# Kernel optimization log

Measured on AMD Instinct MI355X. Metric: run time of the kernel, lower is better.

The kernel has to match this reference:

```python
import jax, jax.numpy as jnp
import numpy as np

E = 8        # num_experts
D_IN = 512   # num_inputs
H = 256      # num_neurons_expert
T = 64       # num_neurons_tower
B = 16384    # batch


def setup_inputs() -> dict:
    key = jax.random.key(0)
    ks = jax.random.split(key, 7)
    s_in = 1.0 / np.sqrt(D_IN)
    s_h = 1.0 / np.sqrt(H)
    return {
        "xv": jax.random.normal(ks[0], (B, D_IN), dtype=jnp.float32),
        # expert weights stacked: torch Linear weight is (out,in) -> (E, H, D_IN)
        "We": jax.random.uniform(ks[1], (E, H, D_IN), jnp.float32, -s_in, s_in),
        "be": jax.random.uniform(ks[2], (E, H), jnp.float32, -s_in, s_in),
        "Wg": jax.random.uniform(ks[3], (E, D_IN), jnp.float32, -s_in, s_in),
        "bg": jax.random.uniform(ks[4], (E,), jnp.float32, -s_in, s_in),
        "Wt": jax.random.uniform(ks[5], (T, H), jnp.float32, -s_h, s_h),
        "bt": jax.random.uniform(ks[6], (T,), jnp.float32, -s_h, s_h),
    }


def reference(xv, We, be, Wg, bg, Wt, bt):
    # All experts as one batched GEMM: [B,D] x [E,H,D] -> [B,E,H]
    experts = jax.nn.relu(jnp.einsum("bd,ehd->beh", xv, We) + be[None, :, :])
    # Dropout is identity in eval mode.
    gate = jax.nn.softmax(xv @ Wg.T + bg, axis=1)            # [B,E]
    combined = jnp.einsum("beh,be->bh", experts, gate)        # [B,H]
    out = jax.nn.sigmoid(combined @ Wt.T + bt)                # [B,T]
    return out
```

## Files before the change

kernel.cpp:

```cpp
#include <hip/hip_runtime.h>
#include <hip/hip_bf16.h>
#include <stdint.h>

typedef unsigned short u16;
typedef __bf16 bf16x8 __attribute__((ext_vector_type(8)));
typedef float f32x4 __attribute__((ext_vector_type(4)));


__device__ __forceinline__ void glds16(const void* g, void* l) {
  __builtin_amdgcn_global_load_lds(
      (const __attribute__((address_space(1))) unsigned int*)g,
      (__attribute__((address_space(3))) unsigned int*)l, 16, 0, 0);
}

__device__ __forceinline__ u16 f2bf(float f) {
  unsigned int u = __builtin_bit_cast(unsigned int, f);
  u += 0x7fffu + ((u >> 16) & 1u);
  return (u16)(u >> 16);
}

__global__ __launch_bounds__(256) void prep_w(
    const float* __restrict__ We, const float* __restrict__ Wt,
    const float* __restrict__ Wg,
    u16* __restrict__ We_bf, u16* __restrict__ Wt_bf,
    u16* __restrict__ Wg_hi, u16* __restrict__ Wg_lo) {
  const int bx = blockIdx.x;
  if (bx < 520) {
    const float* src; u16* dst;
    if (bx < 512) { int base = bx * 2048 + threadIdx.x * 8; src = We + base; dst = We_bf + base; }
    else { int base = (bx - 512) * 2048 + threadIdx.x * 8; src = Wt + base; dst = Wt_bf + base; }
    float4 a = *(const float4*)src;
    float4 b = *(const float4*)(src + 4);
    uint4 o;
    o.x = (unsigned)f2bf(a.x) | ((unsigned)f2bf(a.y) << 16);
    o.y = (unsigned)f2bf(a.z) | ((unsigned)f2bf(a.w) << 16);
    o.z = (unsigned)f2bf(b.x) | ((unsigned)f2bf(b.y) << 16);
    o.w = (unsigned)f2bf(b.z) | ((unsigned)f2bf(b.w) << 16);
    *(uint4*)dst = o;
  } else {
    int base = (bx - 520) * 2048 + threadIdx.x * 8;
    float x[8];
    float4 a = *(const float4*)(Wg + base);
    float4 b = *(const float4*)(Wg + base + 4);
    x[0]=a.x; x[1]=a.y; x[2]=a.z; x[3]=a.w; x[4]=b.x; x[5]=b.y; x[6]=b.z; x[7]=b.w;
    u16 h[8], l[8];
#pragma unroll
    for (int j = 0; j < 8; j++) {
      h[j] = f2bf(x[j]);
      float hf = __builtin_bit_cast(float, ((unsigned)h[j]) << 16);
      l[j] = f2bf(x[j] - hf);
    }
    uint4 oh, ol;
    oh.x = (unsigned)h[0] | ((unsigned)h[1] << 16);
    oh.y = (unsigned)h[2] | ((unsigned)h[3] << 16);
    oh.z = (unsigned)h[4] | ((unsigned)h[5] << 16);
    oh.w = (unsigned)h[6] | ((unsigned)h[7] << 16);
    ol.x = (unsigned)l[0] | ((unsigned)l[1] << 16);
    ol.y = (unsigned)l[2] | ((unsigned)l[3] << 16);
    ol.z = (unsigned)l[4] | ((unsigned)l[5] << 16);
    ol.w = (unsigned)l[6] | ((unsigned)l[7] << 16);
    *(uint4*)(Wg_hi + base) = oh;
    *(uint4*)(Wg_lo + base) = ol;
  }
}

__device__ __forceinline__ void stage_chunk(const u16* __restrict__ We_bf,
                                            u16* ldsbuf, int t, int tid) {
  const int e_ = t >> 3, kc_ = t & 7;
  const u16* src = We_bf + (e_ << 17) + (kc_ << 6);
#pragma unroll
  for (int r = 0; r < 8; r++) {
    int gi = r * 256 + tid;
    int n = gi >> 3, s = gi & 7;
    int g = s ^ (n & 7);
    glds16(src + (n << 9) + (g << 3), ldsbuf + (gi << 3));
  }
}

__global__ __launch_bounds__(256, 2) void moe_main(
    const float* __restrict__ xv, const u16* __restrict__ We_bf,
    const float* __restrict__ be, const float* __restrict__ bg,
    const u16* __restrict__ Wg_hi, const u16* __restrict__ Wg_lo,
    const u16* __restrict__ Wt_bf, const float* __restrict__ bt,
    float* __restrict__ out) {
  __shared__ u16 lds[36864];
  float* beL = (float*)&lds[32768];

  const int tid = threadIdx.x;
  const int lane = tid & 63;
  const int wid = tid >> 6;
  const int wn = wid;
  const int l15 = lane & 15;
  const int l4 = lane >> 4;
  const int m0 = blockIdx.x << 5;

  stage_chunk(We_bf, lds, 0, tid);
  *(float4*)(beL + (tid << 3)) = *(const float4*)(be + (tid << 3));
  *(float4*)(beL + (tid << 3) + 4) = *(const float4*)(be + (tid << 3) + 4);
  stage_chunk(We_bf, &lds[16384], 1, tid);

  bf16x8 ah[2][16];
  f32x4 g0[2] = {{0.f,0.f,0.f,0.f},{0.f,0.f,0.f,0.f}};
  f32x4 g1[2] = {{0.f,0.f,0.f,0.f},{0.f,0.f,0.f,0.f}};
  f32x4 g2[2] = {{0.f,0.f,0.f,0.f},{0.f,0.f,0.f,0.f}};
  const int esrc = l15 & 7;
#pragma unroll
  for (int mt = 0; mt < 2; mt++) {
#pragma unroll
    for (int ks = 0; ks < 16; ks++) {
      const float* ap = xv + ((m0 + mt * 16 + l15) << 9) + ks * 32 + l4 * 8;
      float4 xa = *(const float4*)ap;
      float4 xb = *(const float4*)(ap + 4);
      float x[8];
      x[0]=xa.x; x[1]=xa.y; x[2]=xa.z; x[3]=xa.w; x[4]=xb.x; x[5]=xb.y; x[6]=xb.z; x[7]=xb.w;
      bf16x8 hv, lv;
#pragma unroll
      for (int j = 0; j < 8; j++) {
        u16 hb_ = f2bf(x[j]);
        float hf = __builtin_bit_cast(float, ((unsigned)hb_) << 16);
        hv[j] = __builtin_bit_cast(__bf16, hb_);
        lv[j] = __builtin_bit_cast(__bf16, f2bf(x[j] - hf));
      }
      ah[mt][ks] = hv;
      bf16x8 wh = *(const bf16x8*)(Wg_hi + (esrc << 9) + ks * 32 + l4 * 8);
      bf16x8 wl = *(const bf16x8*)(Wg_lo + (esrc << 9) + ks * 32 + l4 * 8);
      g0[mt] = __builtin_amdgcn_mfma_f32_16x16x32_bf16(hv, wh, g0[mt], 0, 0, 0);
      g1[mt] = __builtin_amdgcn_mfma_f32_16x16x32_bf16(lv, wh, g1[mt], 0, 0, 0);
      g2[mt] = __builtin_amdgcn_mfma_f32_16x16x32_bf16(hv, wl, g2[mt], 0, 0, 0);
    }
  }
  float gv[2][4];
  {
    float bgv = bg[esrc];
#pragma unroll
    for (int mt = 0; mt < 2; mt++)
#pragma unroll
      for (int i = 0; i < 4; i++) {
        float z = g0[mt][i] + g1[mt][i] + g2[mt][i] + bgv;
        float mx = z;
        mx = fmaxf(mx, __shfl_xor(mx, 1));
        mx = fmaxf(mx, __shfl_xor(mx, 2));
        mx = fmaxf(mx, __shfl_xor(mx, 4));
        float p = __expf(z - mx);
        float s = p;
        s += __shfl_xor(s, 1);
        s += __shfl_xor(s, 2);
        s += __shfl_xor(s, 4);
        gv[mt][i] = p / s;
      }
  }

  f32x4 comb[2][4];
#pragma unroll
  for (int mt = 0; mt < 2; mt++)
#pragma unroll
    for (int nt = 0; nt < 4; nt++) comb[mt][nt] = {0.f, 0.f, 0.f, 0.f};

#pragma unroll 1
  for (int e = 0; e < 8; e++) {
    f32x4 acc[2][4];
#pragma unroll
    for (int mt = 0; mt < 2; mt++)
#pragma unroll
      for (int nt = 0; nt < 4; nt++) acc[mt][nt] = {0.f, 0.f, 0.f, 0.f};

#pragma unroll
    for (int kc = 0; kc < 8; kc++) {
      int t = e * 8 + kc;
      __syncthreads();
      if (t + 1 >= 2 && t + 1 < 64)
        stage_chunk(We_bf, &lds[((t & 1) ^ 1) << 14], t + 1, tid);
      const u16* ldsB = &lds[(t & 1) << 14];
#pragma unroll
      for (int ks = 0; ks < 2; ks++) {
        bf16x8 bfr[4];
#pragma unroll
        for (int nt = 0; nt < 4; nt++) {
          int n = wn * 64 + nt * 16 + l15;
          int g = ks * 4 + l4;
          int slot = g ^ (n & 7);
          bfr[nt] = *(const bf16x8*)&ldsB[(n << 6) + (slot << 3)];
        }
#pragma unroll
        for (int mt = 0; mt < 2; mt++)
#pragma unroll
          for (int nt = 0; nt < 4; nt++)
            acc[mt][nt] = __builtin_amdgcn_mfma_f32_16x16x32_bf16(
                ah[mt][kc * 2 + ks], bfr[nt], acc[mt][nt], 0, 0, 0);
      }
    }
    float bev[4];
#pragma unroll
    for (int nt = 0; nt < 4; nt++)
      bev[nt] = beL[(e << 8) + wn * 64 + nt * 16 + l15];
#pragma unroll
    for (int mt = 0; mt < 2; mt++)
#pragma unroll
      for (int i = 0; i < 4; i++) {
        float g = __shfl(gv[mt][i], (lane & 48) | e);
#pragma unroll
        for (int nt = 0; nt < 4; nt++)
          comb[mt][nt][i] += g * fmaxf(acc[mt][nt][i] + bev[nt], 0.f);
      }
  }

#pragma unroll
  for (int mt = 0; mt < 2; mt++)
#pragma unroll
    for (int i = 0; i < 4; i++) {
      int row = mt * 16 + l4 * 4 + i;
#pragma unroll
      for (int nt = 0; nt < 4; nt++) {
        int col = wn * 64 + nt * 16 + l15;
        __bf16 v = (__bf16)comb[mt][nt][i];
        lds[row * 264 + col] = __builtin_bit_cast(u16, v);
      }
    }
  __syncthreads();
  if (wid < 2) {
    f32x4 tacc[4];
#pragma unroll
    for (int nt = 0; nt < 4; nt++) tacc[nt] = {0.f, 0.f, 0.f, 0.f};
#pragma unroll
    for (int ks = 0; ks < 8; ks++) {
      bf16x8 aT = *(const bf16x8*)&lds[(wid * 16 + l15) * 264 + ks * 32 + l4 * 8];
#pragma unroll
      for (int nt = 0; nt < 4; nt++) {
        bf16x8 bT = *(const bf16x8*)&Wt_bf[(nt * 16 + l15) * 256 + ks * 32 + l4 * 8];
        tacc[nt] = __builtin_amdgcn_mfma_f32_16x16x32_bf16(aT, bT, tacc[nt], 0, 0, 0);
      }
    }
#pragma unroll
    for (int nt = 0; nt < 4; nt++) {
      float btv = bt[nt * 16 + l15];
#pragma unroll
      for (int i = 0; i < 4; i++) {
        int row = m0 + wid * 16 + l4 * 4 + i;
        float v = tacc[nt][i] + btv;
        out[row * 64 + nt * 16 + l15] = 1.f / (1.f + __expf(-v));
      }
    }
  }
}

extern "C" void kernel_launch(void* const* d_in, const int* in_sizes, int n_in,
                              void* d_out, int out_size, void* d_ws, size_t ws_size,
                              hipStream_t stream) {
  const float* xv = (const float*)d_in[0];
  const float* We = (const float*)d_in[1];
  const float* be = (const float*)d_in[2];
  const float* Wg = (const float*)d_in[3];
  const float* bg = (const float*)d_in[4];
  const float* Wt = (const float*)d_in[5];
  const float* bt = (const float*)d_in[6];

  char* ws = (char*)d_ws;
  u16* We_bf = (u16*)ws;
  u16* Wt_bf = (u16*)(ws + 2097152);
  u16* Wg_hi = (u16*)(ws + 2129920);
  u16* Wg_lo = (u16*)(ws + 2138112);

  prep_w<<<522, 256, 0, stream>>>(We, Wt, Wg, We_bf, Wt_bf, Wg_hi, Wg_lo);
  moe_main<<<512, 256, 0, stream>>>(xv, We_bf, be, bg, Wg_hi, Wg_lo, Wt_bf, bt,
                                    (float*)d_out);
}
```

Before: 177.9 us.

## Triple-buffer half-size We chunks with vmcnt barriers and stage A fragments in LDS

Splits each We K-chunk into two 128-row halves and cycles them through a three-slot LDS ring. Full __syncthreads are replaced with s_waitcnt vmcnt(4)+s_barrier, so one chunk's loads stay in flight during compute. The bf16 x fragments (ah[2][16]) move from registers into a swizzled LDS tile written by wave 0, freeing VGPRs for occupancy. In exchange, A operands are now reloaded from LDS every k-step, and be is read from global memory instead of LDS.

Result: faster. 152.7 us (-14.1%).

```diff
diff --git a/kernel.cpp b/kernel.cpp
--- a/kernel.cpp
+++ b/kernel.cpp
@@ -6,6 +6,9 @@
 typedef __bf16 bf16x8 __attribute__((ext_vector_type(8)));
 typedef float f32x4 __attribute__((ext_vector_type(4)));
 
+
+#define BAR_V4 asm volatile("s_waitcnt vmcnt(4)\ns_barrier" ::: "memory")
+#define BAR_V0 asm volatile("s_waitcnt vmcnt(0)\ns_barrier" ::: "memory")
 
 __device__ __forceinline__ void glds16(const void* g, void* l) {
   __builtin_amdgcn_global_load_lds(
@@ -65,15 +68,15 @@
 }
 
 __device__ __forceinline__ void stage_chunk(const u16* __restrict__ We_bf,
-                                            u16* ldsbuf, int t, int tid) {
-  const int e_ = t >> 3, kc_ = t & 7;
-  const u16* src = We_bf + (e_ << 17) + (kc_ << 6);
-#pragma unroll
-  for (int r = 0; r < 8; r++) {
+                                            u16* buf, int t, int tid) {
+  const int e_ = t >> 4, kc_ = (t >> 1) & 7, half_ = t & 1;
+  const u16* src = We_bf + (e_ << 17) + (half_ << 16) + (kc_ << 6);
+#pragma unroll
+  for (int r = 0; r < 4; r++) {
     int gi = r * 256 + tid;
     int n = gi >> 3, s = gi & 7;
     int g = s ^ (n & 7);
-    glds16(src + (n << 9) + (g << 3), ldsbuf + (gi << 3));
+    glds16(src + (n << 9) + (g << 3), buf + (gi << 3));
   }
 }
 
@@ -83,8 +86,7 @@
     const u16* __restrict__ Wg_hi, const u16* __restrict__ Wg_lo,
     const u16* __restrict__ Wt_bf, const float* __restrict__ bt,
     float* __restrict__ out) {
-  __shared__ u16 lds[36864];
-  float* beL = (float*)&lds[32768];
+  __shared__ u16 lds[40960];
 
   const int tid = threadIdx.x;
   const int lane = tid & 63;
@@ -94,12 +96,9 @@
   const int l4 = lane >> 4;
   const int m0 = blockIdx.x << 5;
 
-  stage_chunk(We_bf, lds, 0, tid);
-  *(float4*)(beL + (tid << 3)) = *(const float4*)(be + (tid << 3));
-  *(float4*)(beL + (tid << 3) + 4) = *(const float4*)(be + (tid << 3) + 4);
-  stage_chunk(We_bf, &lds[16384], 1, tid);
-
-  bf16x8 ah[2][16];
+  stage_chunk(We_bf, &lds[16384], 0, tid);
+  stage_chunk(We_bf, &lds[16384 + 8192], 1, tid);
+
   f32x4 g0[2] = {{0.f,0.f,0.f,0.f},{0.f,0.f,0.f,0.f}};
   f32x4 g1[2] = {{0.f,0.f,0.f,0.f},{0.f,0.f,0.f,0.f}};
   f32x4 g2[2] = {{0.f,0.f,0.f,0.f},{0.f,0.f,0.f,0.f}};
@@ -108,7 +107,8 @@
   for (int mt = 0; mt < 2; mt++) {
 #pragma unroll
     for (int ks = 0; ks < 16; ks++) {
-      const float* ap = xv + ((m0 + mt * 16 + l15) << 9) + ks * 32 + l4 * 8;
+      const int row = mt * 16 + l15;
+      const float* ap = xv + ((m0 + row) << 9) + ks * 32 + l4 * 8;
       float4 xa = *(const float4*)ap;
       float4 xb = *(const float4*)(ap + 4);
       float x[8];
@@ -121,7 +121,11 @@
         hv[j] = __builtin_bit_cast(__bf16, hb_);
         lv[j] = __builtin_bit_cast(__bf16, f2bf(x[j] - hf));
       }
-      ah[mt][ks] = hv;
+      if (wid == 0) {
+        int gA = ks * 4 + l4;
+        int slotA = (gA & ~7) | ((gA & 7) ^ (row & 7));
+        *(bf16x8*)&lds[(row << 9) + (slotA << 3)] = hv;
+      }
       bf16x8 wh = *(const bf16x8*)(Wg_hi + (esrc << 9) + ks * 32 + l4 * 8);
       bf16x8 wl = *(const bf16x8*)(Wg_lo + (esrc << 9) + ks * 32 + l4 * 8);
       g0[mt] = __builtin_amdgcn_mfma_f32_16x16x32_bf16(hv, wh, g0[mt], 0, 0, 0);
@@ -149,6 +153,7 @@
         gv[mt][i] = p / s;
       }
   }
+  asm volatile("s_waitcnt lgkmcnt(0)\ns_barrier" ::: "memory");
 
   f32x4 comb[2][4];
 #pragma unroll
@@ -156,6 +161,7 @@
 #pragma unroll
     for (int nt = 0; nt < 4; nt++) comb[mt][nt] = {0.f, 0.f, 0.f, 0.f};
 
+  int bcur = 0;
 #pragma unroll 1
   for (int e = 0; e < 8; e++) {
     f32x4 acc[2][4];
@@ -166,53 +172,66 @@
 
 #pragma unroll
     for (int kc = 0; kc < 8; kc++) {
-      int t = e * 8 + kc;
-      __syncthreads();
-      if (t + 1 >= 2 && t + 1 < 64)
-        stage_chunk(We_bf, &lds[((t & 1) ^ 1) << 14], t + 1, tid);
-      const u16* ldsB = &lds[(t & 1) << 14];
-#pragma unroll
-      for (int ks = 0; ks < 2; ks++) {
-        bf16x8 bfr[4];
-#pragma unroll
-        for (int nt = 0; nt < 4; nt++) {
-          int n = wn * 64 + nt * 16 + l15;
-          int g = ks * 4 + l4;
-          int slot = g ^ (n & 7);
-          bfr[nt] = *(const bf16x8*)&ldsB[(n << 6) + (slot << 3)];
+      bf16x8 af[2][2];
+#pragma unroll
+      for (int mt = 0; mt < 2; mt++)
+#pragma unroll
+        for (int ks = 0; ks < 2; ks++) {
+          int gA = (kc * 2 + ks) * 4 + l4;
+          int row = mt * 16 + l15;
+          int slotA = (gA & ~7) | ((gA & 7) ^ (row & 7));
+          af[mt][ks] = *(const bf16x8*)&lds[(row << 9) + (slotA << 3)];
         }
 #pragma unroll
-        for (int mt = 0; mt < 2; mt++)
-#pragma unroll
-          for (int nt = 0; nt < 4; nt++)
-            acc[mt][nt] = __builtin_amdgcn_mfma_f32_16x16x32_bf16(
-                ah[mt][kc * 2 + ks], bfr[nt], acc[mt][nt], 0, 0, 0);
+      for (int half = 0; half < 2; half++) {
+        if (kc == 7 && e == 7 && half == 1) { BAR_V0; } else { BAR_V4; }
+        int t2 = e * 16 + kc * 2 + half + 2;
+        int bstage = bcur >= 1 ? bcur - 1 : 2;
+        if (t2 < 128)
+          stage_chunk(We_bf, &lds[16384 + (bstage << 13)], t2, tid);
+        const u16* Bb = &lds[16384 + (bcur << 13)];
+#pragma unroll
+        for (int ks = 0; ks < 2; ks++) {
+#pragma unroll
+          for (int ntl = 0; ntl < 2; ntl++) {
+            int n = wn * 32 + ntl * 16 + l15;
+            int gB = ks * 4 + l4;
+            int slot = gB ^ (n & 7);
+            bf16x8 bfr = *(const bf16x8*)&Bb[(n << 6) + (slot << 3)];
+#pragma unroll
+            for (int mt = 0; mt < 2; mt++)
+              acc[mt][half * 2 + ntl] = __builtin_amdgcn_mfma_f32_16x16x32_bf16(
+                  af[mt][ks], bfr, acc[mt][half * 2 + ntl], 0, 0, 0);
+          }
+        }
+        bcur = bcur == 2 ? 0 : bcur + 1;
       }
     }
     float bev[4];
 #pragma unroll
-    for (int nt = 0; nt < 4; nt++)
-      bev[nt] = beL[(e << 8) + wn * 64 + nt * 16 + l15];
+    for (int j = 0; j < 4; j++)
+      bev[j] = be[(e << 8) + (j >> 1) * 128 + wn * 32 + (j & 1) * 16 + l15];
 #pragma unroll
     for (int mt = 0; mt < 2; mt++)
 #pragma unroll
       for (int i = 0; i < 4; i++) {
         float g = __shfl(gv[mt][i], (lane & 48) | e);
 #pragma unroll
-        for (int nt = 0; nt < 4; nt++)
-          comb[mt][nt][i] += g * fmaxf(acc[mt][nt][i] + bev[nt], 0.f);
-      }
-  }
-
+        for (int j = 0; j < 4; j++)
+          comb[mt][j][i] += g * fmaxf(acc[mt][j][i] + bev[j], 0.f);
+      }
+  }
+
+  __syncthreads();
 #pragma unroll
   for (int mt = 0; mt < 2; mt++)
 #pragma unroll
     for (int i = 0; i < 4; i++) {
       int row = mt * 16 + l4 * 4 + i;
 #pragma unroll
-      for (int nt = 0; nt < 4; nt++) {
-        int col = wn * 64 + nt * 16 + l15;
-        __bf16 v = (__bf16)comb[mt][nt][i];
+      for (int j = 0; j < 4; j++) {
+        int col = (j >> 1) * 128 + wn * 32 + (j & 1) * 16 + l15;
+        __bf16 v = (__bf16)comb[mt][j][i];
         lds[row * 264 + col] = __builtin_bit_cast(u16, v);
       }
     }
```

## Load expert weights directly from global and keep activations in LDS

Applied to the files above, without the earlier changes.

Drops the double-buffered LDS staging of bf16 expert weights through global_load_lds. Each wave now reads its B fragments straight from global (L2-cached) memory. The bf16 activation tile moves from registers into a swizzled LDS buffer written by wave 0, and the expert bias is read from global instead of LDS. This removes the per-chunk __syncthreads and shrinks LDS and register use, which could raise occupancy. The cost is uncoalesced, latency-exposed global loads of weights inside the MFMA loop.

Result: slower. 222.5 us (+25.1%).

```diff
diff --git a/kernel.cpp b/kernel.cpp
--- a/kernel.cpp
+++ b/kernel.cpp
@@ -6,12 +6,6 @@
 typedef __bf16 bf16x8 __attribute__((ext_vector_type(8)));
 typedef float f32x4 __attribute__((ext_vector_type(4)));
 
-
-__device__ __forceinline__ void glds16(const void* g, void* l) {
-  __builtin_amdgcn_global_load_lds(
-      (const __attribute__((address_space(1))) unsigned int*)g,
-      (__attribute__((address_space(3))) unsigned int*)l, 16, 0, 0);
-}
 
 __device__ __forceinline__ u16 f2bf(float f) {
   unsigned int u = __builtin_bit_cast(unsigned int, f);
@@ -64,27 +58,13 @@
   }
 }
 
-__device__ __forceinline__ void stage_chunk(const u16* __restrict__ We_bf,
-                                            u16* ldsbuf, int t, int tid) {
-  const int e_ = t >> 3, kc_ = t & 7;
-  const u16* src = We_bf + (e_ << 17) + (kc_ << 6);
-#pragma unroll
-  for (int r = 0; r < 8; r++) {
-    int gi = r * 256 + tid;
-    int n = gi >> 3, s = gi & 7;
-    int g = s ^ (n & 7);
-    glds16(src + (n << 9) + (g << 3), ldsbuf + (gi << 3));
-  }
-}
-
 __global__ __launch_bounds__(256, 2) void moe_main(
     const float* __restrict__ xv, const u16* __restrict__ We_bf,
     const float* __restrict__ be, const float* __restrict__ bg,
     const u16* __restrict__ Wg_hi, const u16* __restrict__ Wg_lo,
     const u16* __restrict__ Wt_bf, const float* __restrict__ bt,
     float* __restrict__ out) {
-  __shared__ u16 lds[36864];
-  float* beL = (float*)&lds[32768];
+  __shared__ u16 lds[16384];
 
   const int tid = threadIdx.x;
   const int lane = tid & 63;
@@ -94,12 +74,6 @@
   const int l4 = lane >> 4;
   const int m0 = blockIdx.x << 5;
 
-  stage_chunk(We_bf, lds, 0, tid);
-  *(float4*)(beL + (tid << 3)) = *(const float4*)(be + (tid << 3));
-  *(float4*)(beL + (tid << 3) + 4) = *(const float4*)(be + (tid << 3) + 4);
-  stage_chunk(We_bf, &lds[16384], 1, tid);
-
-  bf16x8 ah[2][16];
   f32x4 g0[2] = {{0.f,0.f,0.f,0.f},{0.f,0.f,0.f,0.f}};
   f32x4 g1[2] = {{0.f,0.f,0.f,0.f},{0.f,0.f,0.f,0.f}};
   f32x4 g2[2] = {{0.f,0.f,0.f,0.f},{0.f,0.f,0.f,0.f}};
@@ -108,7 +82,8 @@
   for (int mt = 0; mt < 2; mt++) {
 #pragma unroll
     for (int ks = 0; ks < 16; ks++) {
-      const float* ap = xv + ((m0 + mt * 16 + l15) << 9) + ks * 32 + l4 * 8;
+      const int row = mt * 16 + l15;
+      const float* ap = xv + ((m0 + row) << 9) + ks * 32 + l4 * 8;
       float4 xa = *(const float4*)ap;
       float4 xb = *(const float4*)(ap + 4);
       float x[8];
@@ -121,7 +96,11 @@
         hv[j] = __builtin_bit_cast(__bf16, hb_);
         lv[j] = __builtin_bit_cast(__bf16, f2bf(x[j] - hf));
       }
-      ah[mt][ks] = hv;
+      if (wid == 0) {
+        int gA = ks * 4 + l4;
+        int slotA = (gA & ~7) | ((gA & 7) ^ (row & 7));
+        *(bf16x8*)&lds[(row << 9) + (slotA << 3)] = hv;
+      }
       bf16x8 wh = *(const bf16x8*)(Wg_hi + (esrc << 9) + ks * 32 + l4 * 8);
       bf16x8 wl = *(const bf16x8*)(Wg_lo + (esrc << 9) + ks * 32 + l4 * 8);
       g0[mt] = __builtin_amdgcn_mfma_f32_16x16x32_bf16(hv, wh, g0[mt], 0, 0, 0);
@@ -149,6 +128,7 @@
         gv[mt][i] = p / s;
       }
   }
+  __syncthreads();
 
   f32x4 comb[2][4];
 #pragma unroll
@@ -164,35 +144,27 @@
 #pragma unroll
       for (int nt = 0; nt < 4; nt++) acc[mt][nt] = {0.f, 0.f, 0.f, 0.f};
 
-#pragma unroll
-    for (int kc = 0; kc < 8; kc++) {
-      int t = e * 8 + kc;
-      __syncthreads();
-      if (t + 1 >= 2 && t + 1 < 64)
-        stage_chunk(We_bf, &lds[((t & 1) ^ 1) << 14], t + 1, tid);
-      const u16* ldsB = &lds[(t & 1) << 14];
-#pragma unroll
-      for (int ks = 0; ks < 2; ks++) {
-        bf16x8 bfr[4];
-#pragma unroll
-        for (int nt = 0; nt < 4; nt++) {
-          int n = wn * 64 + nt * 16 + l15;
-          int g = ks * 4 + l4;
-          int slot = g ^ (n & 7);
-          bfr[nt] = *(const bf16x8*)&ldsB[(n << 6) + (slot << 3)];
-        }
-#pragma unroll
-        for (int mt = 0; mt < 2; mt++)
-#pragma unroll
-          for (int nt = 0; nt < 4; nt++)
-            acc[mt][nt] = __builtin_amdgcn_mfma_f32_16x16x32_bf16(
-                ah[mt][kc * 2 + ks], bfr[nt], acc[mt][nt], 0, 0, 0);
+    const u16* Be = We_bf + (e << 17) + ((wn * 64 + l15) << 9) + l4 * 8;
+#pragma unroll
+    for (int kc = 0; kc < 16; kc++) {
+      bf16x8 af0, af1;
+      {
+        int gA = kc * 4 + l4;
+        int sl = (gA & ~7) | ((gA & 7) ^ (l15 & 7));
+        af0 = *(const bf16x8*)&lds[(l15 << 9) + (sl << 3)];
+        af1 = *(const bf16x8*)&lds[((16 + l15) << 9) + (sl << 3)];
+      }
+#pragma unroll
+      for (int nt = 0; nt < 4; nt++) {
+        bf16x8 bfr = *(const bf16x8*)(Be + (nt << 13) + kc * 32);
+        acc[0][nt] = __builtin_amdgcn_mfma_f32_16x16x32_bf16(af0, bfr, acc[0][nt], 0, 0, 0);
+        acc[1][nt] = __builtin_amdgcn_mfma_f32_16x16x32_bf16(af1, bfr, acc[1][nt], 0, 0, 0);
       }
     }
     float bev[4];
 #pragma unroll
     for (int nt = 0; nt < 4; nt++)
-      bev[nt] = beL[(e << 8) + wn * 64 + nt * 16 + l15];
+      bev[nt] = be[(e << 8) + wn * 64 + nt * 16 + l15];
 #pragma unroll
     for (int mt = 0; mt < 2; mt++)
 #pragma unroll
@@ -204,6 +176,7 @@
       }
   }
 
+  __syncthreads();
 #pragma unroll
   for (int mt = 0; mt < 2; mt++)
 #pragma unroll
```

## Retile MoE kernel to 64-row blocks split over H halves with partial tower outputs

Applied to the files above, without the earlier changes.

Each block now handles 64 rows and one half of the expert hidden dimension, using a 2x2 wave grid. The bf16 activations are staged into swizzled LDS instead of being held in registers. Weight chunks are single-buffered with two barriers per chunk, replacing the previous double-buffered prefetch. Tower partial sums from the two H halves go to a workspace, and a new finish kernel adds them with the bias and applies the sigmoid. The aim is more reuse of each staged weight chunk across rows and less register pressure, at the cost of losing load/compute overlap, an extra launch and extra global traffic for the partials.

Result: faster. 157.3 us (-11.6%).

```diff
diff --git a/kernel.cpp b/kernel.cpp
--- a/kernel.cpp
+++ b/kernel.cpp
@@ -6,6 +6,7 @@
 typedef __bf16 bf16x8 __attribute__((ext_vector_type(8)));
 typedef float f32x4 __attribute__((ext_vector_type(4)));
 
+#define LDS_B_OFF 32768
 
 __device__ __forceinline__ void glds16(const void* g, void* l) {
   __builtin_amdgcn_global_load_lds(
@@ -64,42 +65,25 @@
   }
 }
 
-__device__ __forceinline__ void stage_chunk(const u16* __restrict__ We_bf,
-                                            u16* ldsbuf, int t, int tid) {
-  const int e_ = t >> 3, kc_ = t & 7;
-  const u16* src = We_bf + (e_ << 17) + (kc_ << 6);
-#pragma unroll
-  for (int r = 0; r < 8; r++) {
-    int gi = r * 256 + tid;
-    int n = gi >> 3, s = gi & 7;
-    int g = s ^ (n & 7);
-    glds16(src + (n << 9) + (g << 3), ldsbuf + (gi << 3));
-  }
-}
-
 __global__ __launch_bounds__(256, 2) void moe_main(
     const float* __restrict__ xv, const u16* __restrict__ We_bf,
     const float* __restrict__ be, const float* __restrict__ bg,
     const u16* __restrict__ Wg_hi, const u16* __restrict__ Wg_lo,
-    const u16* __restrict__ Wt_bf, const float* __restrict__ bt,
-    float* __restrict__ out) {
-  __shared__ u16 lds[36864];
-  float* beL = (float*)&lds[32768];
-
+    const u16* __restrict__ Wt_bf, float* __restrict__ part) {
+  __shared__ u16 lds[40960];
+
+  const int bx = ((blockIdx.x & 7) << 6) | (blockIdx.x >> 3);
+  const int mb = bx >> 1;
+  const int hb = bx & 1;
+  const int m0 = mb << 6;
   const int tid = threadIdx.x;
   const int lane = tid & 63;
   const int wid = tid >> 6;
-  const int wn = wid;
+  const int wm = wid >> 1;
+  const int wn = wid & 1;
   const int l15 = lane & 15;
   const int l4 = lane >> 4;
-  const int m0 = blockIdx.x << 5;
-
-  stage_chunk(We_bf, lds, 0, tid);
-  *(float4*)(beL + (tid << 3)) = *(const float4*)(be + (tid << 3));
-  *(float4*)(beL + (tid << 3) + 4) = *(const float4*)(be + (tid << 3) + 4);
-  stage_chunk(We_bf, &lds[16384], 1, tid);
-
-  bf16x8 ah[2][16];
+
   f32x4 g0[2] = {{0.f,0.f,0.f,0.f},{0.f,0.f,0.f,0.f}};
   f32x4 g1[2] = {{0.f,0.f,0.f,0.f},{0.f,0.f,0.f,0.f}};
   f32x4 g2[2] = {{0.f,0.f,0.f,0.f},{0.f,0.f,0.f,0.f}};
@@ -108,7 +92,8 @@
   for (int mt = 0; mt < 2; mt++) {
 #pragma unroll
     for (int ks = 0; ks < 16; ks++) {
-      const float* ap = xv + ((m0 + mt * 16 + l15) << 9) + ks * 32 + l4 * 8;
+      const int row = wm * 32 + mt * 16 + l15;
+      const float* ap = xv + ((m0 + row) << 9) + ks * 32 + l4 * 8;
       float4 xa = *(const float4*)ap;
       float4 xb = *(const float4*)(ap + 4);
       float x[8];
@@ -121,7 +106,11 @@
         hv[j] = __builtin_bit_cast(__bf16, hb_);
         lv[j] = __builtin_bit_cast(__bf16, f2bf(x[j] - hf));
       }
-      ah[mt][ks] = hv;
+      if (wn == 0) {
+        int gA = ks * 4 + l4;
+        int slotA = (gA & ~7) | ((gA & 7) ^ (row & 7));
+        *(bf16x8*)&lds[(row << 9) + (slotA << 3)] = hv;
+      }
       bf16x8 wh = *(const bf16x8*)(Wg_hi + (esrc << 9) + ks * 32 + l4 * 8);
       bf16x8 wl = *(const bf16x8*)(Wg_lo + (esrc << 9) + ks * 32 + l4 * 8);
       g0[mt] = __builtin_amdgcn_mfma_f32_16x16x32_bf16(hv, wh, g0[mt], 0, 0, 0);
@@ -156,7 +145,6 @@
 #pragma unroll
     for (int nt = 0; nt < 4; nt++) comb[mt][nt] = {0.f, 0.f, 0.f, 0.f};
 
-#pragma unroll 1
   for (int e = 0; e < 8; e++) {
     f32x4 acc[2][4];
 #pragma unroll
@@ -164,37 +152,48 @@
 #pragma unroll
       for (int nt = 0; nt < 4; nt++) acc[mt][nt] = {0.f, 0.f, 0.f, 0.f};
 
-#pragma unroll
+    const u16* Wb = We_bf + (e << 17) + (hb << 16);
     for (int kc = 0; kc < 8; kc++) {
-      int t = e * 8 + kc;
       __syncthreads();
-      if (t + 1 >= 2 && t + 1 < 64)
-        stage_chunk(We_bf, &lds[((t & 1) ^ 1) << 14], t + 1, tid);
-      const u16* ldsB = &lds[(t & 1) << 14];
+#pragma unroll
+      for (int r = 0; r < 4; r++) {
+        int gi = r * 256 + tid;
+        int n = gi >> 3, s = gi & 7;
+        int g = s ^ (n & 7);
+        glds16(Wb + (n << 9) + (kc << 6) + (g << 3), &lds[LDS_B_OFF + (gi << 3)]);
+      }
+      __syncthreads();
 #pragma unroll
       for (int ks = 0; ks < 2; ks++) {
-        bf16x8 bfr[4];
+        bf16x8 af[2], bfr[4];
+#pragma unroll
+        for (int mt = 0; mt < 2; mt++) {
+          int row = wm * 32 + mt * 16 + l15;
+          int gk = kc * 8 + ks * 4 + l4;
+          int slot = (gk & ~7) | ((gk & 7) ^ (row & 7));
+          af[mt] = *(const bf16x8*)&lds[(row << 9) + (slot << 3)];
+        }
 #pragma unroll
         for (int nt = 0; nt < 4; nt++) {
           int n = wn * 64 + nt * 16 + l15;
-          int g = ks * 4 + l4;
-          int slot = g ^ (n & 7);
-          bfr[nt] = *(const bf16x8*)&ldsB[(n << 6) + (slot << 3)];
+          int gB = ks * 4 + l4;
+          int slot = gB ^ (n & 7);
+          bfr[nt] = *(const bf16x8*)&lds[LDS_B_OFF + (n << 6) + (slot << 3)];
         }
 #pragma unroll
         for (int mt = 0; mt < 2; mt++)
 #pragma unroll
           for (int nt = 0; nt < 4; nt++)
             acc[mt][nt] = __builtin_amdgcn_mfma_f32_16x16x32_bf16(
-                ah[mt][kc * 2 + ks], bfr[nt], acc[mt][nt], 0, 0, 0);
+                af[mt], bfr[nt], acc[mt][nt], 0, 0, 0);
       }
     }
     float bev[4];
 #pragma unroll
     for (int nt = 0; nt < 4; nt++)
-      bev[nt] = beL[(e << 8) + wn * 64 + nt * 16 + l15];
-#pragma unroll
-    for (int mt = 0; mt < 2; mt++)
+      bev[nt] = be[(e << 8) + (hb << 7) + wn * 64 + nt * 16 + l15];
+#pragma unroll
+    for (int mt = 0; mt < 2; mt++) {
 #pragma unroll
       for (int i = 0; i < 4; i++) {
         float g = __shfl(gv[mt][i], (lane & 48) | e);
@@ -202,45 +201,60 @@
         for (int nt = 0; nt < 4; nt++)
           comb[mt][nt][i] += g * fmaxf(acc[mt][nt][i] + bev[nt], 0.f);
       }
-  }
-
+    }
+  }
+
+  __syncthreads();
 #pragma unroll
   for (int mt = 0; mt < 2; mt++)
 #pragma unroll
     for (int i = 0; i < 4; i++) {
-      int row = mt * 16 + l4 * 4 + i;
+      int row = wm * 32 + mt * 16 + l4 * 4 + i;
 #pragma unroll
       for (int nt = 0; nt < 4; nt++) {
         int col = wn * 64 + nt * 16 + l15;
         __bf16 v = (__bf16)comb[mt][nt][i];
-        lds[row * 264 + col] = __builtin_bit_cast(u16, v);
+        lds[row * 136 + col] = __builtin_bit_cast(u16, v);
       }
     }
   __syncthreads();
-  if (wid < 2) {
-    f32x4 tacc[4];
-#pragma unroll
-    for (int nt = 0; nt < 4; nt++) tacc[nt] = {0.f, 0.f, 0.f, 0.f};
-#pragma unroll
-    for (int ks = 0; ks < 8; ks++) {
-      bf16x8 aT = *(const bf16x8*)&lds[(wid * 16 + l15) * 264 + ks * 32 + l4 * 8];
-#pragma unroll
-      for (int nt = 0; nt < 4; nt++) {
-        bf16x8 bT = *(const bf16x8*)&Wt_bf[(nt * 16 + l15) * 256 + ks * 32 + l4 * 8];
-        tacc[nt] = __builtin_amdgcn_mfma_f32_16x16x32_bf16(aT, bT, tacc[nt], 0, 0, 0);
-      }
-    }
+  f32x4 tacc[4];
+#pragma unroll
+  for (int nt = 0; nt < 4; nt++) tacc[nt] = {0.f, 0.f, 0.f, 0.f};
+  const u16* WtB = Wt_bf + (hb << 7);
+#pragma unroll
+  for (int kc = 0; kc < 4; kc++) {
+    int ko = kc * 32 + l4 * 8;
+    bf16x8 aT = *(const bf16x8*)&lds[(wid * 16 + l15) * 136 + ko];
 #pragma unroll
     for (int nt = 0; nt < 4; nt++) {
-      float btv = bt[nt * 16 + l15];
-#pragma unroll
-      for (int i = 0; i < 4; i++) {
-        int row = m0 + wid * 16 + l4 * 4 + i;
-        float v = tacc[nt][i] + btv;
-        out[row * 64 + nt * 16 + l15] = 1.f / (1.f + __expf(-v));
-      }
-    }
-  }
+      bf16x8 bT = *(const bf16x8*)&WtB[(nt * 16 + l15) * 256 + ko];
+      tacc[nt] = __builtin_amdgcn_mfma_f32_16x16x32_bf16(aT, bT, tacc[nt], 0, 0, 0);
+    }
+  }
+  float* pout = part + hb * 1048576;
+#pragma unroll
+  for (int nt = 0; nt < 4; nt++)
+#pragma unroll
+    for (int i = 0; i < 4; i++) {
+      int grow = m0 + wid * 16 + l4 * 4 + i;
+      pout[grow * 64 + nt * 16 + l15] = tacc[nt][i];
+    }
+}
+
+__global__ __launch_bounds__(256) void finish_kernel(
+    const float* __restrict__ part, const float* __restrict__ bt,
+    float* __restrict__ out) {
+  const int idx = (blockIdx.x * 256 + threadIdx.x) << 2;
+  float4 a = *(const float4*)(part + idx);
+  float4 b = *(const float4*)(part + 1048576 + idx);
+  float4 c = *(const float4*)(bt + (idx & 63));
+  float4 r;
+  r.x = 1.f / (1.f + __expf(-(a.x + b.x + c.x)));
+  r.y = 1.f / (1.f + __expf(-(a.y + b.y + c.y)));
+  r.z = 1.f / (1.f + __expf(-(a.z + b.z + c.z)));
+  r.w = 1.f / (1.f + __expf(-(a.w + b.w + c.w)));
+  *(float4*)(out + idx) = r;
 }
 
 extern "C" void kernel_launch(void* const* d_in, const int* in_sizes, int n_in,
@@ -259,8 +273,9 @@
   u16* Wt_bf = (u16*)(ws + 2097152);
   u16* Wg_hi = (u16*)(ws + 2129920);
   u16* Wg_lo = (u16*)(ws + 2138112);
+  float* part = (float*)(ws + 2146304);
 
   prep_w<<<522, 256, 0, stream>>>(We, Wt, Wg, We_bf, Wt_bf, Wg_hi, Wg_lo);
-  moe_main<<<512, 256, 0, stream>>>(xv, We_bf, be, bg, Wg_hi, Wg_lo, Wt_bf, bt,
-                                    (float*)d_out);
-}
+  moe_main<<<512, 256, 0, stream>>>(xv, We_bf, be, bg, Wg_hi, Wg_lo, Wt_bf, part);
+  finish_kernel<<<1024, 256, 0, stream>>>(part, bt, (float*)d_out);
+}
```
